# Optimization experiments

Hardware: AMD Instinct MI355X
Metric: run time of the kernel (lower is better)

The kernel has to match this reference:

```python
import jax, jax.numpy as jnp
import numpy as np
from jax import lax

B, C, H, W = 2, 256, 64, 64
CI = C // 2           # inter_channels = 128
CH = CI // 2          # key/query channels = 64
EPS = 1e-5


def conv1x1(x, w, b):
    # x: [B,C,H,W], w: [O,C], b: [O]
    return jnp.einsum('oc,bchw->bohw', w, x) + b[None, :, None, None]


def bn(x, g, be, m, v):
    inv = (g / jnp.sqrt(v + EPS))[None, :, None, None]
    return (x - m[None, :, None, None]) * inv + be[None, :, None, None]


def setup_inputs() -> dict:
    key = jax.random.key(0)
    ks = jax.random.split(key, 40)
    r = lambda i, shape, sc=0.05: jax.random.normal(ks[i], shape, dtype=jnp.float32) * sc
    u = lambda i, shape: jax.random.uniform(ks[i], shape, dtype=jnp.float32, minval=0.5, maxval=1.5)
    return {
        'q': jax.random.normal(ks[0], (B, C, H, W), dtype=jnp.float32),
        's': jax.random.normal(ks[1], (B, C, H, W), dtype=jnp.float32),
        'scale': jnp.full((1,), 0.3, dtype=jnp.float32),
        'w_v': r(2, (CI, C)), 'b_v': r(3, (CI,)),
        'w_k1': r(4, (CH, C)), 'b_k1': r(5, (CH,)),
        'w_q1': r(6, (CH, C)), 'b_q1': r(7, (CH,)),
        'w_k2': r(8, (CH, C)), 'b_k2': r(9, (CH,)),
        'w_q2': r(10, (CH, C)), 'b_q2': r(11, (CH,)),
        'w_ts': r(12, (CI, C)), 'b_ts': r(13, (CI,)),
        'g_ts': u(14, (CI,)), 'be_ts': r(15, (CI,)), 'm_ts': r(16, (CI,)), 'v_ts': u(17, (CI,)),
        'w_tq': r(18, (CI, C)), 'b_tq': r(19, (CI,)),
        'g_tq': u(20, (CI,)), 'be_tq': r(21, (CI,)), 'm_tq': r(22, (CI,)), 'v_tq': u(23, (CI,)),
        'w_cat': r(24, (CI, 2 * CI, 3, 3)),
        'g_cat': u(25, (CI,)), 'be_cat': r(26, (CI,)), 'm_cat': r(27, (CI,)), 'v_cat': u(28, (CI,)),
    }


def reference(q, s, scale, w_v, b_v, w_k1, b_k1, w_q1, b_q1, w_k2, b_k2, w_q2, b_q2,
              w_ts, b_ts, g_ts, be_ts, m_ts, v_ts,
              w_tq, b_tq, g_tq, be_tq, m_tq, v_tq,
              w_cat, g_cat, be_cat, m_cat, v_cat):
    b_, _, h, w = q.shape
    n = h * w
    # values: [B, N, CI]
    v_q = conv1x1(q, w_v, b_v).reshape(b_, CI, n).transpose(0, 2, 1)
    v_s = conv1x1(s, w_v, b_v).reshape(b_, CI, n).transpose(0, 2, 1)
    # concatenated keys/queries: [B, CI, N]
    k_x = jnp.concatenate([conv1x1(q, w_k1, b_k1), conv1x1(s, w_k2, b_k2)], axis=1).reshape(b_, CI, n)
    q_x = jnp.concatenate([conv1x1(q, w_q1, b_q1), conv1x1(s, w_q2, b_q2)], axis=1).reshape(b_, CI, n)
    # affinity: [B, N, N]
    A_s = jnp.einsum('bcn,bcm->bnm', k_x, q_x)
    attn_s = jax.nn.softmax(A_s, axis=-1)
    attn_q = jax.nn.softmax(jnp.transpose(A_s, (0, 2, 1)), axis=-1)
    # p_s: [B, N, CI] -> [B, CI, H, W]
    p_s = jnp.einsum('bnm,bmc->bnc', attn_s, v_s).transpose(0, 2, 1).reshape(b_, CI, h, w)
    s_t = bn(conv1x1(s, w_ts, b_ts), g_ts, be_ts, m_ts, v_ts)
    q_t = bn(conv1x1(q, w_tq, b_tq), g_tq, be_tq, m_tq, v_tq)
    E_s = scale[0] * p_s + s_t
    q_s_ = jnp.einsum('bnm,bmc->bnc', attn_q, v_q).transpose(0, 2, 1).reshape(b_, CI, h, w)
    E_q = scale[0] * q_s_ + q_t
    cat = jnp.concatenate([E_q, E_s], axis=1)
    conv = lax.conv_general_dilated(cat, w_cat, (1, 1), 'SAME',
                                    dimension_numbers=('NCHW', 'OIHW', 'NCHW'))
    cpam = jax.nn.relu(bn(conv, g_cat, be_cat, m_cat, v_cat))
    return (cpam, E_q, E_s)
```

## Files before the change

kernel.cpp:

```cpp
#include <hip/hip_runtime.h>
#include <hip/hip_bf16.h>

#define NPIX 4096
#define NCH  256
#define CI   128
#define EPS  1e-5f
#define SOFF 20.0f

typedef unsigned short u16;
typedef __attribute__((ext_vector_type(8))) short short8;
typedef __attribute__((ext_vector_type(4))) float f32x4;

__device__ __forceinline__ float bfu2f(u16 u) {
    union { unsigned int i; float f; } x; x.i = ((unsigned int)u) << 16; return x.f;
}
__device__ __forceinline__ u16 f2bfu(float f) {
    union { float ff; unsigned int i; } x; x.ff = f;
    unsigned int r = x.i + 0x7FFFu + ((x.i >> 16) & 1u);
    return (u16)(r >> 16);
}

__device__ __forceinline__ void gload16(const u16* g, u16* l) {
    __builtin_amdgcn_global_load_lds(
        (const __attribute__((address_space(1))) unsigned int*)g,
        (__attribute__((address_space(3))) unsigned int*)l,
        16, 0, 0);
}

__global__ __launch_bounds__(256) void prep_kernel(
    const float* __restrict__ w_v,
    const float* __restrict__ w_k1, const float* __restrict__ w_q1,
    const float* __restrict__ w_k2, const float* __restrict__ w_q2,
    const float* __restrict__ w_ts, const float* __restrict__ w_tq,
    u16* __restrict__ Wbf,
    const float* __restrict__ w_cat, u16* __restrict__ wT)
{
    const int bx = blockIdx.x;
    if (bx < 768) {
        int idx = bx * 256 + threadIdx.x;
        int src = idx / 98304;
        int r   = idx - src * 98304;
        int o   = r >> 8, c = r & 255;
        float v;
        if (o < 128)      v = w_v[(size_t)o * 256 + c];
        else if (o < 192) v = (src ? w_k2 : w_k1)[(size_t)(o - 128) * 256 + c];
        else if (o < 256) v = (src ? w_q2 : w_q1)[(size_t)(o - 192) * 256 + c];
        else              v = (src ? w_ts : w_tq)[(size_t)(o - 256) * 256 + c];
        Wbf[idx] = f2bfu(v);
    } else {
        int co = bx - 768;
        const float* srcb = w_cat + (size_t)co * 2304;
        u16* dstb = wT + (size_t)co * 2304;
        for (int t = threadIdx.x; t < 2304; t += 256) {
            int ic = t / 9, tap = t - ic * 9;
            dstb[tap * 256 + ic] = f2bfu(srcb[t]);
        }
    }
}

__global__ __launch_bounds__(256) void proj2_kernel(
    const float* __restrict__ xq, const float* __restrict__ xs,
    const u16* __restrict__ Wbf,
    const float* __restrict__ b_v,
    const float* __restrict__ b_k1, const float* __restrict__ b_q1,
    const float* __restrict__ b_k2, const float* __restrict__ b_q2,
    const float* __restrict__ b_ts, const float* __restrict__ g_ts,
    const float* __restrict__ be_ts, const float* __restrict__ m_ts,
    const float* __restrict__ v_ts,
    const float* __restrict__ b_tq, const float* __restrict__ g_tq,
    const float* __restrict__ be_tq, const float* __restrict__ m_tq,
    const float* __restrict__ v_tq,
    u16* __restrict__ kT, u16* __restrict__ qT,
    u16* __restrict__ vq, u16* __restrict__ vs,
    u16* __restrict__ tq, u16* __restrict__ ts)
{
    __shared__ u16 Xs[64 * 264];
    __shared__ u16 KQ[64 * 136];

    const int tid  = threadIdx.x;
    const int lane = tid & 63;
    const int wid  = tid >> 6;
    const int l16  = lane & 15;
    const int quad = lane >> 4;

    const int n0  = blockIdx.x * 64;
    const int bz  = blockIdx.z;
    const int b   = bz >> 1, src = bz & 1;

    const float* xg = (src ? xs : xq) + (size_t)b * NCH * NPIX + n0;
    #pragma unroll
    for (int k0 = 0; k0 < 64; k0 += 16) {
        float v[16];
        #pragma unroll
        for (int k = 0; k < 16; ++k) {
            int idx = tid + (k0 + k) * 256;
            int c = idx >> 6, n = idx & 63;
            v[k] = xg[(size_t)c * NPIX + n];
        }
        #pragma unroll
        for (int k = 0; k < 16; ++k) {
            int idx = tid + (k0 + k) * 256;
            int c = idx >> 6, n = idx & 63;
            Xs[n * 264 + c] = f2bfu(v[k]);
        }
    }
    __syncthreads();

    const u16* W = Wbf + (size_t)src * 384 * 256;
    const int o0w = wid * 96;
    const float* bk = src ? b_k2 : b_k1;
    const float* bq = src ? b_q2 : b_q1;
    const float* bt = src ? b_ts : b_tq;

    f32x4 acc[24];
    #pragma unroll
    for (int ot = 0; ot < 6; ++ot) {
        int ob = o0w + ot * 16 + quad * 4;
        const float* bp;
        if (ob < 128)      bp = b_v + ob;
        else if (ob < 192) bp = bk + (ob - 128);
        else if (ob < 256) bp = bq + (ob - 192);
        else               bp = bt + (ob - 256);
        float4 b4 = *(const float4*)bp;
        f32x4 iv = (f32x4){b4.x, b4.y, b4.z, b4.w};
        #pragma unroll
        for (int pt = 0; pt < 4; ++pt) acc[ot * 4 + pt] = iv;
    }

    #pragma unroll
    for (int kc = 0; kc < 8; ++kc) {
        short8 bfr[4];
        #pragma unroll
        for (int pt = 0; pt < 4; ++pt)
            bfr[pt] = *(const short8*)&Xs[(pt * 16 + l16) * 264 + kc * 32 + quad * 8];
        #pragma unroll
        for (int ot = 0; ot < 6; ++ot) {
            short8 a = *(const short8*)&W[(size_t)(o0w + ot * 16 + l16) * 256 + kc * 32 + quad * 8];
            #pragma unroll
            for (int pt = 0; pt < 4; ++pt)
                acc[ot * 4 + pt] = __builtin_amdgcn_mfma_f32_16x16x32_bf16(a, bfr[pt], acc[ot * 4 + pt], 0, 0, 0);
        }
    }

    #pragma unroll
    for (int ot = 0; ot < 6; ++ot) {
        int ob = o0w + ot * 16;
        #pragma unroll
        for (int pt = 0; pt < 4; ++pt) {
            int px = pt * 16 + l16;
            f32x4 v4 = acc[ot * 4 + pt];
            if (ob < 128) {
                u16* dst = src ? vs : vq;
                #pragma unroll
                for (int r = 0; r < 4; ++r)
                    dst[((size_t)b * CI + ob + quad * 4 + r) * NPIX + n0 + px] = f2bfu(v4[r]);
            } else if (ob < 256) {
                int colb = (ob < 192) ? (ob - 128) : (64 + ob - 192);
                #pragma unroll
                for (int r = 0; r < 4; ++r)
                    KQ[px * 136 + colb + quad * 4 + r] = f2bfu(v4[r]);
            } else {
                const float* g  = src ? g_ts  : g_tq;
                const float* be = src ? be_ts : be_tq;
                const float* mm = src ? m_ts  : m_tq;
                const float* vv = src ? v_ts  : v_tq;
                u16* dst = src ? ts : tq;
                #pragma unroll
                for (int r = 0; r < 4; ++r) {
                    int oc = ob - 256 + quad * 4 + r;
                    float inv = g[oc] * rsqrtf(vv[oc] + EPS);
                    dst[((size_t)b * CI + oc) * NPIX + n0 + px] =
                        f2bfu((v4[r] - mm[oc]) * inv + be[oc]);
                }
            }
        }
    }
    __syncthreads();

    const int chb = src ? 64 : 0;
    #pragma unroll
    for (int u = 0; u < 4; ++u) {
        int idx = tid + u * 256;
        int px = idx >> 4, oct = idx & 15;
        uint4 val = *(const uint4*)&KQ[px * 136 + oct * 8];
        if (oct < 8)
            *(uint4*)&kT[((size_t)b * NPIX + n0 + px) * CI + chb + oct * 8] = val;
        else
            *(uint4*)&qT[((size_t)b * NPIX + n0 + px) * CI + chb + (oct - 8) * 8] = val;
    }
}

#define AKS_OFF 0
#define AVT_OFF 8192
#define APS_OFF 16384
#define ASMEM_U16 18944

__global__ __launch_bounds__(256, 4) void attn_kernel(
    const u16* __restrict__ kT, const u16* __restrict__ qT,
    const u16* __restrict__ vq, const u16* __restrict__ vs,
    u16* __restrict__ Opart, float* __restrict__ Lpart, int nseg)
{
    __shared__ __align__(16) u16 smem[ASMEM_U16];
    u16* Ps = smem + APS_OFF;

    const int tid  = threadIdx.x;
    const int lane = tid & 63;
    const int wid  = tid >> 6;
    const int l16  = lane & 15;
    const int quad = lane >> 4;
    const int strip = wid * 16;

    const int nt = blockIdx.x;
    const int n0 = nt * 64;
    const int at = blockIdx.y;
    const int z  = blockIdx.z;
    const int b  = z / nseg;
    const int seg = z - b * nseg;

    const u16* Qg = at ? qT : kT;
    const u16* Kg = at ? kT : qT;
    const u16* Vg = at ? vq : vs;

    short8 qf[4];
    {
        const u16* Qb = Qg + ((size_t)b * NPIX + n0 + strip + l16) * CI;
        #pragma unroll
        for (int kc = 0; kc < 4; ++kc)
            qf[kc] = *(const short8*)&Qb[kc * 32 + quad * 8];
    }

    f32x4 o[8];
    #pragma unroll
    for (int ct = 0; ct < 8; ++ct) o[ct] = (f32x4){0.f, 0.f, 0.f, 0.f};
    float L = 0.f;

    const u16* KgB = Kg + (size_t)b * NPIX * CI;
    const u16* VgB = Vg + (size_t)b * CI * NPIX;

    const int mt0 = seg * (128 / nseg);
    const int mt1 = mt0 + (128 / nseg);

    #define ISSUE_TILE(buf, m0_)                                              \
    {                                                                         \
        u16* kb_ = smem + AKS_OFF + (buf) * 4096;                             \
        u16* vb_ = smem + AVT_OFF + (buf) * 4096;                             \
        _Pragma("unroll")                                                     \
        for (int k = 0; k < 2; ++k) {                                         \
            int sb  = k * 256 + wid * 64;                                     \
            int idx = sb + lane;                                              \
            int row = idx >> 4, segp = idx & 15;                              \
            int segg = segp ^ (row & 15);                                     \
            gload16(KgB + (size_t)((m0_) + row) * CI + segg * 8, kb_ + sb * 8); \
        }                                                                     \
        _Pragma("unroll")                                                     \
        for (int k = 0; k < 2; ++k) {                                         \
            int sb  = k * 256 + wid * 64;                                     \
            int idx = sb + lane;                                              \
            int c = idx >> 2, sgp = idx & 3;                                  \
            int sgg = sgp ^ ((c ^ (c >> 2)) & 3);                             \
            gload16(VgB + (size_t)c * NPIX + (m0_) + sgg * 8, vb_ + sb * 8);  \
        }                                                                     \
    }

    int cur = 0;
    ISSUE_TILE(0, mt0 * 32);

    for (int mt = mt0; mt < mt1; ++mt) {
        __syncthreads();
        if (mt + 1 < mt1) ISSUE_TILE(1 - cur, (mt + 1) * 32);

        const u16* Ks = smem + AKS_OFF + cur * 4096;
        const u16* Vt = smem + AVT_OFF + cur * 4096;

        f32x4 sv[2];
        __builtin_amdgcn_s_setprio(1);
        #pragma unroll
        for (int m2 = 0; m2 < 2; ++m2) {
            f32x4 c = (f32x4){0.f, 0.f, 0.f, 0.f};
            #pragma unroll
            for (int kc = 0; kc < 4; ++kc) {
                int s = kc * 4 + quad;
                short8 kf = *(const short8*)&Ks[(m2 * 16 + l16) * 128 + ((s ^ l16) * 8)];
                c = __builtin_amdgcn_mfma_f32_16x16x32_bf16(kf, qf[kc], c, 0, 0, 0);
            }
            sv[m2] = c;
        }
        __builtin_amdgcn_s_setprio(0);

        float Lsum = 0.f;
        u16* myPs = Ps + (strip + l16) * 40;
        #pragma unroll
        for (int m2 = 0; m2 < 2; ++m2) {
            float p0 = __expf(sv[m2][0] - SOFF);
            float p1 = __expf(sv[m2][1] - SOFF);
            float p2 = __expf(sv[m2][2] - SOFF);
            float p3 = __expf(sv[m2][3] - SOFF);
            Lsum += (p0 + p1) + (p2 + p3);
            unsigned int r0, r1;
            asm("v_cvt_pk_bf16_f32 %0, %1, %2" : "=v"(r0) : "v"(p0), "v"(p1));
            asm("v_cvt_pk_bf16_f32 %0, %1, %2" : "=v"(r1) : "v"(p2), "v"(p3));
            uint2 pk; pk.x = r0; pk.y = r1;
            *(uint2*)&myPs[m2 * 16 + quad * 4] = pk;
        }
        Lsum += __shfl_xor(Lsum, 16);
        Lsum += __shfl_xor(Lsum, 32);
        L += Lsum;

        short8 ap = *(const short8*)&Ps[(strip + l16) * 40 + quad * 8];
        __builtin_amdgcn_s_setprio(1);
        #pragma unroll
        for (int ct = 0; ct < 8; ++ct) {
            int cc = ct * 16 + l16;
            int fc = (cc ^ (cc >> 2)) & 3;
            short8 bv = *(const short8*)&Vt[cc * 32 + ((quad ^ fc) * 8)];
            o[ct] = __builtin_amdgcn_mfma_f32_16x16x32_bf16(ap, bv, o[ct], 0, 0, 0);
        }
        __builtin_amdgcn_s_setprio(0);
        cur ^= 1;
    }

    const size_t tile = (((size_t)(at * 2 + b) * 64 + nt) * nseg + seg);
    u16* Ob = Opart + tile * 8192;
    #pragma unroll
    for (int r = 0; r < 4; ++r) {
        int row = strip + quad * 4 + r;
        #pragma unroll
        for (int ct = 0; ct < 8; ++ct)
            Ob[row * 128 + ct * 16 + l16] = f2bfu(o[ct][r]);
    }
    if (quad == 0)
        Lpart[tile * 64 + strip + l16] = L;
    #undef ISSUE_TILE
}

__global__ __launch_bounds__(256) void attn_combine_kernel(
    const u16* __restrict__ Opart, const float* __restrict__ Lpart,
    const u16* __restrict__ tq, const u16* __restrict__ ts,
    const float* __restrict__ scale_p,
    float* __restrict__ out, u16* __restrict__ Ebf, int nseg)
{
    __shared__ float Of[128 * 68];
    __shared__ float invL[64];

    const int tid = threadIdx.x;
    const int nt = blockIdx.x;
    const int n0 = nt * 64;
    const int at = blockIdx.y;
    const int b  = blockIdx.z;

    const u16* Tg = at ? tq : ts;
    float* outE   = out + (size_t)(at ? 1 : 2) * 1048576;
    const int ch0 = at ? 0 : 128;
    const size_t tbase = ((size_t)(at * 2 + b) * 64 + nt) * nseg;

    if (tid < 64) {
        float Lg = 0.f;
        for (int s = 0; s < nseg; ++s) Lg += Lpart[(tbase + s) * 64 + tid];
        invL[tid] = 1.f / Lg;
    }
    __syncthreads();

    #pragma unroll
    for (int k = 0; k < 4; ++k) {
        int idx = tid + k * 256;
        int row = idx >> 4, oct = idx & 15;
        float m[8] = {0.f, 0.f, 0.f, 0.f, 0.f, 0.f, 0.f, 0.f};
        for (int s = 0; s < nseg; ++s) {
            union { uint4 v; u16 u[8]; } pk;
            pk.v = *(const uint4*)&Opart[(tbase + s) * 8192 + row * 128 + oct * 8];
            #pragma unroll
            for (int j = 0; j < 8; ++j) m[j] += bfu2f(pk.u[j]);
        }
        float w = invL[row];
        #pragma unroll
        for (int j = 0; j < 8; ++j)
            Of[(oct * 8 + j) * 68 + row] = m[j] * w;
    }
    __syncthreads();

    float scale = *scale_p;
    const u16* Tb = Tg + (size_t)b * CI * NPIX + n0;
    float* Ob = outE + (size_t)b * CI * NPIX + n0;
    for (int idx = tid; idx < 128 * 64; idx += 256) {
        int c = idx >> 6, r = idx & 63;
        float v = scale * Of[c * 68 + r] + bfu2f(Tb[(size_t)c * NPIX + r]);
        Ob[(size_t)c * NPIX + r] = v;
        Ebf[((size_t)b * NPIX + n0 + r) * NCH + ch0 + c] = f2bfu(v);
    }
}

#define CXT_STR 40

__global__ __launch_bounds__(256) void conv_kernel(
    const u16* __restrict__ Ebf,
    const u16* __restrict__ wT,
    const float* __restrict__ g_cat, const float* __restrict__ be_cat,
    const float* __restrict__ m_cat, const float* __restrict__ v_cat,
    float* __restrict__ out)
{
    __shared__ u16 XtW[4][3 * 34 * CXT_STR];

    const int tid  = threadIdx.x;
    const int lane = tid & 63;
    const int wid  = tid >> 6;
    const int l16  = lane & 15;
    const int quad = lane >> 4;

    const int h    = blockIdx.x;
    const int coff = blockIdx.y * 32;
    const int b    = blockIdx.z;

    const int cot = wid >> 1;
    const int pxt = (wid & 1) * 2;
    const int gc0 = pxt * 16 - 1;

    f32x4 acc[2];
    #pragma unroll
    for (int j = 0; j < 2; ++j) acc[j] = (f32x4){0.f, 0.f, 0.f, 0.f};

    const u16* Eb = Ebf + (size_t)b * NPIX * NCH;
    u16* Xw = &XtW[wid][0];
    const int cobase = coff + cot * 16 + l16;

    for (int icc = 0; icc < 8; ++icc) {
        const int ic0 = icc * 32;

        short8 wfrag[9];
        #pragma unroll
        for (int tap = 0; tap < 9; ++tap)
            wfrag[tap] = *(const short8*)&wT[((size_t)cobase * 9 + tap) * 256 + ic0 + quad * 8];

        for (int u = lane; u < 408; u += 64) {
            int part = u & 3, xe = u >> 2;
            int dh = xe / 34, x = xe - dh * 34;
            int gr = h + dh - 1, gc = gc0 + x;
            uint4 val = make_uint4(0u, 0u, 0u, 0u);
            if ((unsigned)gr < 64u && (unsigned)gc < 64u)
                val = *(const uint4*)&Eb[((size_t)gr * 64 + gc) * NCH + ic0 + part * 8];
            *(uint4*)&Xw[(dh * 34 + x) * CXT_STR + part * 8] = val;
        }

        #pragma unroll
        for (int tap = 0; tap < 9; ++tap) {
            const int dh = tap / 3, dw = tap % 3;
            short8 bf[2];
            #pragma unroll
            for (int j = 0; j < 2; ++j) {
                int x = j * 16 + l16 + dw;
                bf[j] = *(const short8*)&Xw[(dh * 34 + x) * CXT_STR + quad * 8];
            }
            #pragma unroll
            for (int j = 0; j < 2; ++j)
                acc[j] = __builtin_amdgcn_mfma_f32_16x16x32_bf16(wfrag[tap], bf[j], acc[j], 0, 0, 0);
        }
    }

    #pragma unroll
    for (int r = 0; r < 4; ++r) {
        int co = coff + cot * 16 + quad * 4 + r;
        float inv = g_cat[co] * rsqrtf(v_cat[co] + EPS);
        float mm  = m_cat[co];
        float be  = be_cat[co];
        #pragma unroll
        for (int j = 0; j < 2; ++j) {
            int wcol = (pxt + j) * 16 + l16;
            float v = (acc[j][r] - mm) * inv + be;
            out[((size_t)b * CI + co) * NPIX + h * 64 + wcol] = fmaxf(v, 0.f);
        }
    }
}

extern "C" void kernel_launch(void* const* d_in, const int* in_sizes, int n_in,
                              void* d_out, int out_size, void* d_ws, size_t ws_size,
                              hipStream_t stream)
{
    const float* q     = (const float*)d_in[0];
    const float* s     = (const float*)d_in[1];
    const float* scale = (const float*)d_in[2];
    const float* w_v   = (const float*)d_in[3];
    const float* b_v   = (const float*)d_in[4];
    const float* w_k1  = (const float*)d_in[5];
    const float* b_k1  = (const float*)d_in[6];
    const float* w_q1  = (const float*)d_in[7];
    const float* b_q1  = (const float*)d_in[8];
    const float* w_k2  = (const float*)d_in[9];
    const float* b_k2  = (const float*)d_in[10];
    const float* w_q2  = (const float*)d_in[11];
    const float* b_q2  = (const float*)d_in[12];
    const float* w_ts  = (const float*)d_in[13];
    const float* b_ts  = (const float*)d_in[14];
    const float* g_ts  = (const float*)d_in[15];
    const float* be_ts = (const float*)d_in[16];
    const float* m_ts  = (const float*)d_in[17];
    const float* v_ts  = (const float*)d_in[18];
    const float* w_tq  = (const float*)d_in[19];
    const float* b_tq  = (const float*)d_in[20];
    const float* g_tq  = (const float*)d_in[21];
    const float* be_tq = (const float*)d_in[22];
    const float* m_tq  = (const float*)d_in[23];
    const float* v_tq  = (const float*)d_in[24];
    const float* w_cat = (const float*)d_in[25];
    const float* g_cat = (const float*)d_in[26];
    const float* be_cat= (const float*)d_in[27];
    const float* m_cat = (const float*)d_in[28];
    const float* v_cat = (const float*)d_in[29];

    float* out = (float*)d_out;
    u16* ws = (u16*)d_ws;
    const size_t SZ = (size_t)2 * CI * NPIX;
    u16* kT  = ws;
    u16* qT  = kT + SZ;
    u16* vq  = qT + SZ;
    u16* vs  = vq + SZ;
    u16* tq  = vs + SZ;
    u16* ts  = tq + SZ;
    u16* Wbf = ts + SZ;
    u16* B   = Wbf + 196608;
    u16* Ebf = B;
    u16* wTc = B + 2097152;
    u16* Opart = wTc + 294912;

    const size_t fixed_u16 = 6 * SZ + 196608 + 2097152 + 294912;
    int nseg = 1;
    {
        size_t need4 = (fixed_u16 + (size_t)4 * 2097152) * 2 + (size_t)4 * 131072;
        size_t need2 = (fixed_u16 + (size_t)2 * 2097152) * 2 + (size_t)2 * 131072;
        if (ws_size >= need4)      nseg = 4;
        else if (ws_size >= need2) nseg = 2;
    }
    float* Lpart = (float*)(Opart + (size_t)nseg * 256 * 8192);

    dim3 blk(256);
    hipLaunchKernelGGL(prep_kernel, dim3(896), blk, 0, stream,
                       w_v, w_k1, w_q1, w_k2, w_q2, w_ts, w_tq, Wbf, w_cat, wTc);
    hipLaunchKernelGGL(proj2_kernel, dim3(64, 1, 4), blk, 0, stream,
                       q, s, Wbf, b_v, b_k1, b_q1, b_k2, b_q2,
                       b_ts, g_ts, be_ts, m_ts, v_ts,
                       b_tq, g_tq, be_tq, m_tq, v_tq,
                       kT, qT, vq, vs, tq, ts);
    hipLaunchKernelGGL(attn_kernel, dim3(64, 2, 2 * nseg), blk, 0, stream,
                       kT, qT, vq, vs, Opart, Lpart, nseg);
    hipLaunchKernelGGL(attn_combine_kernel, dim3(64, 2, 2), blk, 0, stream,
                       Opart, Lpart, tq, ts, scale, out, Ebf, nseg);
    hipLaunchKernelGGL(conv_kernel, dim3(64, 4, 2), blk, 0, stream,
                       Ebf, wTc, g_cat, be_cat, m_cat, v_cat, out);
}
```

Baseline: 241.4 us.

## Switch attention kernel to 32x32x16 MFMA with register-shuffled P, 2 waves/block

```diff
diff --git a/kernel.cpp b/kernel.cpp
--- a/kernel.cpp
+++ b/kernel.cpp
@@ -10,6 +10,7 @@
 typedef unsigned short u16;
 typedef __attribute__((ext_vector_type(8))) short short8;
 typedef __attribute__((ext_vector_type(4))) float f32x4;
+typedef __attribute__((ext_vector_type(16))) float f32x16;
 
 __device__ __forceinline__ float bfu2f(u16 u) {
     union { unsigned int i; float f; } x; x.i = ((unsigned int)u) << 16; return x.f;
@@ -192,23 +193,20 @@
 
 #define AKS_OFF 0
 #define AVT_OFF 8192
-#define APS_OFF 16384
-#define ASMEM_U16 18944
-
-__global__ __launch_bounds__(256, 4) void attn_kernel(
+#define ASMEM_U16 16384
+
+__global__ __launch_bounds__(128) void attn_kernel(
     const u16* __restrict__ kT, const u16* __restrict__ qT,
     const u16* __restrict__ vq, const u16* __restrict__ vs,
     u16* __restrict__ Opart, float* __restrict__ Lpart, int nseg)
 {
     __shared__ __align__(16) u16 smem[ASMEM_U16];
-    u16* Ps = smem + APS_OFF;
 
     const int tid  = threadIdx.x;
     const int lane = tid & 63;
-    const int wid  = tid >> 6;
-    const int l16  = lane & 15;
-    const int quad = lane >> 4;
-    const int strip = wid * 16;
+    const int qh   = tid >> 6;
+    const int l32  = lane & 31;
+    const int h    = lane >> 5;
 
     const int nt = blockIdx.x;
     const int n0 = nt * 64;
@@ -221,17 +219,19 @@
     const u16* Kg = at ? kT : qT;
     const u16* Vg = at ? vq : vs;
 
-    short8 qf[4];
+    short8 qf[8];
     {
-        const u16* Qb = Qg + ((size_t)b * NPIX + n0 + strip + l16) * CI;
-        #pragma unroll
-        for (int kc = 0; kc < 4; ++kc)
-            qf[kc] = *(const short8*)&Qb[kc * 32 + quad * 8];
-    }
-
-    f32x4 o[8];
-    #pragma unroll
-    for (int ct = 0; ct < 8; ++ct) o[ct] = (f32x4){0.f, 0.f, 0.f, 0.f};
+        const u16* Qb = Qg + ((size_t)b * NPIX + n0 + qh * 32 + l32) * CI;
+        #pragma unroll
+        for (int kc = 0; kc < 8; ++kc)
+            qf[kc] = *(const short8*)&Qb[kc * 16 + h * 8];
+    }
+
+    f32x16 o[4];
+    #pragma unroll
+    for (int ct = 0; ct < 4; ++ct)
+        #pragma unroll
+        for (int r = 0; r < 16; ++r) o[ct][r] = 0.f;
     float L = 0.f;
 
     const u16* KgB = Kg + (size_t)b * NPIX * CI;
@@ -239,26 +239,28 @@
 
     const int mt0 = seg * (128 / nseg);
     const int mt1 = mt0 + (128 / nseg);
+
+    const int fv = (l32 >> 1) & 3;
 
     #define ISSUE_TILE(buf, m0_)                                              \
     {                                                                         \
         u16* kb_ = smem + AKS_OFF + (buf) * 4096;                             \
         u16* vb_ = smem + AVT_OFF + (buf) * 4096;                             \
         _Pragma("unroll")                                                     \
-        for (int k = 0; k < 2; ++k) {                                         \
-            int sb  = k * 256 + wid * 64;                                     \
+        for (int k = 0; k < 4; ++k) {                                         \
+            int sb  = k * 128 + qh * 64;                                      \
             int idx = sb + lane;                                              \
-            int row = idx >> 4, segp = idx & 15;                              \
-            int segg = segp ^ (row & 15);                                     \
-            gload16(KgB + (size_t)((m0_) + row) * CI + segg * 8, kb_ + sb * 8); \
+            int row = idx >> 4, p = idx & 15;                                 \
+            int pg = p ^ (row & 15);                                          \
+            gload16(KgB + (size_t)((m0_) + row) * CI + pg * 8, kb_ + sb * 8); \
         }                                                                     \
         _Pragma("unroll")                                                     \
-        for (int k = 0; k < 2; ++k) {                                         \
-            int sb  = k * 256 + wid * 64;                                     \
+        for (int k = 0; k < 4; ++k) {                                         \
+            int sb  = k * 128 + qh * 64;                                      \
             int idx = sb + lane;                                              \
-            int c = idx >> 2, sgp = idx & 3;                                  \
-            int sgg = sgp ^ ((c ^ (c >> 2)) & 3);                             \
-            gload16(VgB + (size_t)c * NPIX + (m0_) + sgg * 8, vb_ + sb * 8);  \
+            int c = idx >> 2, p = idx & 3;                                    \
+            int pg = p ^ ((c >> 1) & 3);                                      \
+            gload16(VgB + (size_t)c * NPIX + (m0_) + pg * 8, vb_ + sb * 8);   \
         }                                                                     \
     }
 
@@ -272,48 +274,51 @@
         const u16* Ks = smem + AKS_OFF + cur * 4096;
         const u16* Vt = smem + AVT_OFF + cur * 4096;
 
-        f32x4 sv[2];
+        f32x16 c;
+        #pragma unroll
+        for (int r = 0; r < 16; ++r) c[r] = 0.f;
         __builtin_amdgcn_s_setprio(1);
         #pragma unroll
-        for (int m2 = 0; m2 < 2; ++m2) {
-            f32x4 c = (f32x4){0.f, 0.f, 0.f, 0.f};
-            #pragma unroll
-            for (int kc = 0; kc < 4; ++kc) {
-                int s = kc * 4 + quad;
-                short8 kf = *(const short8*)&Ks[(m2 * 16 + l16) * 128 + ((s ^ l16) * 8)];
-                c = __builtin_amdgcn_mfma_f32_16x16x32_bf16(kf, qf[kc], c, 0, 0, 0);
-            }
-            sv[m2] = c;
+        for (int kc = 0; kc < 8; ++kc) {
+            short8 kf = *(const short8*)&Ks[l32 * 128 + (((kc * 2 + h) ^ (l32 & 15)) * 8)];
+            c = __builtin_amdgcn_mfma_f32_32x32x16_bf16(kf, qf[kc], c, 0, 0, 0);
         }
         __builtin_amdgcn_s_setprio(0);
 
+        unsigned int pk[8];
         float Lsum = 0.f;
-        u16* myPs = Ps + (strip + l16) * 40;
-        #pragma unroll
-        for (int m2 = 0; m2 < 2; ++m2) {
-            float p0 = __expf(sv[m2][0] - SOFF);
-            float p1 = __expf(sv[m2][1] - SOFF);
-            float p2 = __expf(sv[m2][2] - SOFF);
-            float p3 = __expf(sv[m2][3] - SOFF);
-            Lsum += (p0 + p1) + (p2 + p3);
-            unsigned int r0, r1;
-            asm("v_cvt_pk_bf16_f32 %0, %1, %2" : "=v"(r0) : "v"(p0), "v"(p1));
-            asm("v_cvt_pk_bf16_f32 %0, %1, %2" : "=v"(r1) : "v"(p2), "v"(p3));
-            uint2 pk; pk.x = r0; pk.y = r1;
-            *(uint2*)&myPs[m2 * 16 + quad * 4] = pk;
-        }
-        Lsum += __shfl_xor(Lsum, 16);
+        #pragma unroll
+        for (int t = 0; t < 8; ++t) {
+            float p0 = __expf(c[2 * t]     - SOFF);
+            float p1 = __expf(c[2 * t + 1] - SOFF);
+            Lsum += p0 + p1;
+            asm("v_cvt_pk_bf16_f32 %0, %1, %2" : "=v"(pk[t]) : "v"(p0), "v"(p1));
+        }
         Lsum += __shfl_xor(Lsum, 32);
         L += Lsum;
 
-        short8 ap = *(const short8*)&Ps[(strip + l16) * 40 + quad * 8];
+        unsigned int pw0 = __shfl_xor(pk[0], 32), pw1 = __shfl_xor(pk[1], 32);
+        unsigned int pw2 = __shfl_xor(pk[2], 32), pw3 = __shfl_xor(pk[3], 32);
+        unsigned int pw4 = __shfl_xor(pk[4], 32), pw5 = __shfl_xor(pk[5], 32);
+        unsigned int pw6 = __shfl_xor(pk[6], 32), pw7 = __shfl_xor(pk[7], 32);
+        union { unsigned int u[4]; short8 s8; } a0, a1;
+        a0.u[0] = h ? pw2 : pk[0];
+        a0.u[1] = h ? pw3 : pk[1];
+        a0.u[2] = h ? pk[2] : pw0;
+        a0.u[3] = h ? pk[3] : pw1;
+        a1.u[0] = h ? pw6 : pk[4];
+        a1.u[1] = h ? pw7 : pk[5];
+        a1.u[2] = h ? pk[6] : pw4;
+        a1.u[3] = h ? pk[7] : pw5;
+
         __builtin_amdgcn_s_setprio(1);
         #pragma unroll
-        for (int ct = 0; ct < 8; ++ct) {
-            int cc = ct * 16 + l16;
-            int fc = (cc ^ (cc >> 2)) & 3;
-            short8 bv = *(const short8*)&Vt[cc * 32 + ((quad ^ fc) * 8)];
-            o[ct] = __builtin_amdgcn_mfma_f32_16x16x32_bf16(ap, bv, o[ct], 0, 0, 0);
+        for (int ct = 0; ct < 4; ++ct) {
+            int ci = ct * 32 + l32;
+            short8 b0 = *(const short8*)&Vt[ci * 32 + (((    h) ^ fv) * 8)];
+            o[ct] = __builtin_amdgcn_mfma_f32_32x32x16_bf16(a0.s8, b0, o[ct], 0, 0, 0);
+            short8 b1 = *(const short8*)&Vt[ci * 32 + (((2 + h) ^ fv) * 8)];
+            o[ct] = __builtin_amdgcn_mfma_f32_32x32x16_bf16(a1.s8, b1, o[ct], 0, 0, 0);
         }
         __builtin_amdgcn_s_setprio(0);
         cur ^= 1;
@@ -322,14 +327,14 @@
     const size_t tile = (((size_t)(at * 2 + b) * 64 + nt) * nseg + seg);
     u16* Ob = Opart + tile * 8192;
     #pragma unroll
-    for (int r = 0; r < 4; ++r) {
-        int row = strip + quad * 4 + r;
-        #pragma unroll
-        for (int ct = 0; ct < 8; ++ct)
-            Ob[row * 128 + ct * 16 + l16] = f2bfu(o[ct][r]);
-    }
-    if (quad == 0)
-        Lpart[tile * 64 + strip + l16] = L;
+    for (int r = 0; r < 16; ++r) {
+        int row = qh * 32 + (r & 3) + 8 * (r >> 2) + 4 * h;
+        #pragma unroll
+        for (int ct = 0; ct < 4; ++ct)
+            Ob[row * 128 + ct * 32 + l32] = f2bfu(o[ct][r]);
+    }
+    if (h == 0)
+        Lpart[tile * 64 + qh * 32 + l32] = L;
     #undef ISSUE_TILE
 }
 
@@ -538,7 +543,7 @@
                        b_ts, g_ts, be_ts, m_ts, v_ts,
                        b_tq, g_tq, be_tq, m_tq, v_tq,
                        kT, qT, vq, vs, tq, ts);
-    hipLaunchKernelGGL(attn_kernel, dim3(64, 2, 2 * nseg), blk, 0, stream,
+    hipLaunchKernelGGL(attn_kernel, dim3(64, 2, 2 * nseg), dim3(128), 0, stream,
                        kT, qT, vq, vs, Opart, Lpart, nseg);
     hipLaunchKernelGGL(attn_combine_kernel, dim3(64, 2, 2), blk, 0, stream,
                        Opart, Lpart, tq, ts, scale, out, Ebf, nseg);
```

Result: no change. 245.4 us (+1.6%).
